# Kernel tuning notes

Hardware: AMD Instinct MI355X
Metric: run time of the kernel (lower is better)

The kernel has to match this reference:

```python
import jax, jax.numpy as jnp
import numpy as np

I, H = 4, 64


def setup_inputs() -> dict:
    key = jax.random.key(0)
    ks = jax.random.split(key, 7)
    s_ih = 1.0 / np.sqrt(H)
    return {
        "x": jax.random.normal(ks[0], (8192, 512, I), dtype=jnp.float32),
        "W_ih": jax.random.uniform(ks[1], (4 * H, I), minval=-s_ih, maxval=s_ih, dtype=jnp.float32),
        "W_hh": jax.random.uniform(ks[2], (4 * H, H), minval=-s_ih, maxval=s_ih, dtype=jnp.float32),
        "b_ih": jax.random.uniform(ks[3], (4 * H,), minval=-s_ih, maxval=s_ih, dtype=jnp.float32),
        "b_hh": jax.random.uniform(ks[4], (4 * H,), minval=-s_ih, maxval=s_ih, dtype=jnp.float32),
        "W_fc": jax.random.uniform(ks[5], (1, H), minval=-s_ih, maxval=s_ih, dtype=jnp.float32),
        "b_fc": jax.random.uniform(ks[6], (1,), minval=-s_ih, maxval=s_ih, dtype=jnp.float32),
    }


def _lstm_last_hidden(x, W_ih, W_hh, b_ih, b_hh):
    # x: [B, T, I] batch_first; PyTorch gate order: i, f, g, o
    B = x.shape[0]
    # Precompute input projections for all timesteps in one GEMM: [T, B, 4H]
    xg = jnp.einsum('bti,gi->tbg', x, W_ih) + (b_ih + b_hh)

    def step(carry, xg_t):
        h, c = carry
        gates = xg_t + h @ W_hh.T  # [B, 4H]
        i, f, g, o = jnp.split(gates, 4, axis=-1)
        i = jax.nn.sigmoid(i)
        f = jax.nn.sigmoid(f)
        g = jnp.tanh(g)
        o = jax.nn.sigmoid(o)
        c = f * c + i * g
        h = o * jnp.tanh(c)
        return (h, c), None

    h0 = jnp.zeros((B, W_hh.shape[1]), dtype=x.dtype)
    c0 = jnp.zeros_like(h0)
    (h_n, _), _ = jax.lax.scan(step, (h0, c0), xg)
    return h_n  # [B, H]


def reference(x, W_ih, W_hh, b_ih, b_hh, W_fc, b_fc):
    h_n = _lstm_last_hidden(x, W_ih, W_hh, b_ih, b_hh)
    return h_n @ W_fc.T + b_fc  # [B, 1]
```

## Files before the change

### kernel.cpp

```cpp
#include <hip/hip_runtime.h>


typedef float f32x4 __attribute__((ext_vector_type(4)));
typedef _Float16 f16x8 __attribute__((ext_vector_type(8)));
typedef _Float16 f16x4 __attribute__((ext_vector_type(4)));

#define TSEQ 512
#define IDIM 4
#define BPB 16
#define TCH 32
#define NCH (TSEQ / TCH)
#define L2E 1.44269504088896340736f

#if __has_builtin(__builtin_amdgcn_exp2f)
#define EX2(v) __builtin_amdgcn_exp2f(v)
#else
#define EX2(v) exp2f(v)
#endif
#define RCP(v) __builtin_amdgcn_rcpf(v)

#define STEP_BARRIER() do {                                   \
    asm volatile("s_waitcnt lgkmcnt(0)" ::: "memory");        \
    __builtin_amdgcn_s_barrier();                             \
} while (0)

__global__ __launch_bounds__(256, 2) void lstm_fused(
    const float* __restrict__ x,
    const float* __restrict__ W_ih,
    const float* __restrict__ W_hh,
    const float* __restrict__ b_ih,
    const float* __restrict__ b_hh,
    const float* __restrict__ W_fc,
    const float* __restrict__ b_fc,
    float* __restrict__ out)
{
    __shared__ __align__(16) _Float16 hbuf[2][BPB * 64];
    __shared__ __align__(16) f16x4    xstage[2][BPB][33];

    const int tid  = threadIdx.x;
    const int lane = tid & 63;
    const int wv   = tid >> 6;
    const int b0   = blockIdx.x * BPB;
    const int r    = lane & 15;
    const int g16  = lane >> 4;

    f16x8 bfrag[4][3];
    #pragma unroll
    for (int t4 = 0; t4 < 4; ++t4) {
        const float sc = (t4 == 2) ? 2.0f * L2E : L2E;
        const int g = t4 * 64 + wv * 16 + r;
        #pragma unroll
        for (int ks = 0; ks < 2; ++ks) {
            const float* p = W_hh + g * 64 + ks * 32 + g16 * 8;
            f16x8 f;
            #pragma unroll
            for (int j = 0; j < 8; ++j) f[j] = (_Float16)(p[j] * sc);
            bfrag[t4][ks] = f;
        }
        f16x8 f;
        #pragma unroll
        for (int j = 0; j < 8; ++j) f[j] = (_Float16)0.0f;
        if (g16 == 0) {
            #pragma unroll
            for (int j = 0; j < 4; ++j) f[j] = (_Float16)(W_ih[g * IDIM + j] * sc);
            float biasf = (b_ih[g] + b_hh[g]) * sc;
            _Float16 hi = (_Float16)biasf;
            f[4] = hi;
            f[5] = (_Float16)(biasf - (float)hi);
        }
        bfrag[t4][2] = f;
    }
    const float wfc = W_fc[lane];
    const float bfc = b_fc[0];
    const f32x4 zero4 = {0.f, 0.f, 0.f, 0.f};

    float c_reg[4] = {0.f, 0.f, 0.f, 0.f};
    for (int i = tid; i < BPB * 64; i += 256) hbuf[0][i] = (_Float16)0.0f;

    const int bb0 = tid >> 5, tf = tid & 31;
    const float* xg0 = x + ((size_t)(b0 + bb0)     * TSEQ + tf) * IDIM;
    const float* xg1 = x + ((size_t)(b0 + bb0 + 8) * TSEQ + tf) * IDIM;
    float4 xn0 = *(const float4*)xg0;
    float4 xn1 = *(const float4*)xg1;
    {
        f16x4 s0, s1;
        s0[0] = (_Float16)xn0.x; s0[1] = (_Float16)xn0.y;
        s0[2] = (_Float16)xn0.z; s0[3] = (_Float16)xn0.w;
        s1[0] = (_Float16)xn1.x; s1[1] = (_Float16)xn1.y;
        s1[2] = (_Float16)xn1.z; s1[3] = (_Float16)xn1.w;
        xstage[0][bb0][tf]     = s0;
        xstage[0][bb0 + 8][tf] = s1;
    }
    __syncthreads();
    xn0 = *(const float4*)(xg0 + TCH * IDIM);
    xn1 = *(const float4*)(xg1 + TCH * IDIM);

    if (((blockIdx.x ^ (blockIdx.x >> 8)) & 1) != 0)
        __builtin_amdgcn_s_sleep(13);

    const int hbase = r * 128;
    const int hs0 = ((g16 + 0) << 4) ^ ((r & 7) << 4);
    const int hs1 = ((g16 + 4) << 4) ^ ((r & 7) << 4);
    int hw[4];
    #pragma unroll
    for (int q = 0; q < 4; ++q) {
        const int bat = 4 * g16 + q;
        hw[q] = (bat * 128 + (wv * 16 + r) * 2) ^ ((bat & 7) << 4);
    }
    char* hbB = (char*)&hbuf[0][0];
    const char* xsB = (const char*)&xstage[0][0][0];
    const int xrow = r * 33 * 8;

    auto substep = [&](int t, int P) {
        const char* rb = hbB + P * 2048;
        char*       wb = hbB + (P ^ 1) * 2048;
        f16x8 a0 = *(const f16x8*)(rb + hbase + hs0);
        f16x8 a1 = *(const f16x8*)(rb + hbase + hs1);
        f16x4 xv = *(const f16x4*)(xsB + ((t >> 5) & 1) * 4224 + xrow + (t & 31) * 8);
        f16x8 ax;
        ax[0] = xv[0]; ax[1] = xv[1]; ax[2] = xv[2]; ax[3] = xv[3];
        ax[4] = (_Float16)1.0f; ax[5] = (_Float16)1.0f;
        ax[6] = (_Float16)0.0f; ax[7] = (_Float16)0.0f;

        f32x4 acc[4];
        __builtin_amdgcn_s_setprio(1);
        #pragma unroll
        for (int t4 = 0; t4 < 4; ++t4) {
            f32x4 a;
            a = __builtin_amdgcn_mfma_f32_16x16x32_f16(a0, bfrag[t4][0], zero4, 0, 0, 0);
            a = __builtin_amdgcn_mfma_f32_16x16x32_f16(a1, bfrag[t4][1], a, 0, 0, 0);
            a = __builtin_amdgcn_mfma_f32_16x16x32_f16(ax, bfrag[t4][2], a, 0, 0, 0);
            acc[t4] = a;
        }
        __builtin_amdgcn_s_setprio(0);

        #pragma unroll
        for (int q = 0; q < 4; ++q) {
            float ei = EX2(-acc[0][q]);
            float ef = EX2(-acc[1][q]);
            float eg = EX2(-acc[2][q]);
            float eo = EX2(-acc[3][q]);
            float A  = 1.f + ei, F = 1.f + ef;
            float Gp = 1.f + eg, Gm = 1.f - eg;
            float P2  = A * Gp;
            float num = c_reg[q] * P2 + Gm * F;
            float c   = num * RCP(P2 * F);
            c_reg[q] = c;
            float uc = fminf(fmaxf(c * (2.0f * L2E), -60.f), 60.f);
            float et = EX2(-uc);
            float h  = (1.f - et) * RCP((1.f + eo) * (1.f + et));
            *(_Float16*)(wb + hw[q]) = (_Float16)h;
        }
        STEP_BARRIER();
    };

    for (int t = 0; t < TSEQ; t += 2) {
        if ((t & (TCH - 1)) == 16) {
            const int c = t >> 5;
            if (c + 1 < NCH) {
                f16x4 s0, s1;
                s0[0] = (_Float16)xn0.x; s0[1] = (_Float16)xn0.y;
                s0[2] = (_Float16)xn0.z; s0[3] = (_Float16)xn0.w;
                s1[0] = (_Float16)xn1.x; s1[1] = (_Float16)xn1.y;
                s1[2] = (_Float16)xn1.z; s1[3] = (_Float16)xn1.w;
                f16x4* dst = &xstage[(c + 1) & 1][0][0];
                dst[bb0 * 33 + tf]       = s0;
                dst[(bb0 + 8) * 33 + tf] = s1;
                if (c + 2 < NCH) {
                    xn0 = *(const float4*)(xg0 + (size_t)(c + 2) * TCH * IDIM);
                    xn1 = *(const float4*)(xg1 + (size_t)(c + 2) * TCH * IDIM);
                }
            }
        }
        substep(t,     0);
        substep(t + 1, 1);
    }

    #pragma unroll
    for (int q = 0; q < 4; ++q) {
        const int bat  = wv * 4 + q;
        const int byte = (bat * 128 + lane * 2) ^ ((bat & 7) << 4);
        float hv = (float)*(const _Float16*)(hbB + byte);
        float partial = hv * wfc;
        #pragma unroll
        for (int off = 32; off > 0; off >>= 1)
            partial += __shfl_down(partial, off);
        if (lane == 0) out[b0 + bat] = partial + bfc;
    }
}

extern "C" void kernel_launch(void* const* d_in, const int* in_sizes, int n_in,
                              void* d_out, int out_size, void* d_ws, size_t ws_size,
                              hipStream_t stream) {
    const float* x    = (const float*)d_in[0];
    const float* W_ih = (const float*)d_in[1];
    const float* W_hh = (const float*)d_in[2];
    const float* b_ih = (const float*)d_in[3];
    const float* b_hh = (const float*)d_in[4];
    const float* W_fc = (const float*)d_in[5];
    const float* b_fc = (const float*)d_in[6];
    float* out = (float*)d_out;

    const int B = in_sizes[0] / (TSEQ * IDIM);
    lstm_fused<<<B / BPB, 256, 0, stream>>>(x, W_ih, W_hh, b_ih, b_hh, W_fc, b_fc, out);
}
```

Measured before the change: 323.9 us.

## Replace LDS x staging with per-lane register prefetch ring and pack cell math

Removes the shared-memory x staging buffer and its periodic chunk copy. Each lane now keeps an 8-deep register ring of float4 x values that it loads straight from global memory, prefetching RING steps ahead. The cell-update math is rewritten with 2-wide float vectors so the compiler can emit packed FP32 ops. In exchange, every step issues a global load per lane that four waves make redundantly, register pressure rises, and the upper clamp on the tanh argument is dropped.

```diff
diff --git a/kernel.cpp b/kernel.cpp
--- a/kernel.cpp
+++ b/kernel.cpp
@@ -2,14 +2,13 @@
 
 
 typedef float f32x4 __attribute__((ext_vector_type(4)));
+typedef float f32x2 __attribute__((ext_vector_type(2)));
 typedef _Float16 f16x8 __attribute__((ext_vector_type(8)));
-typedef _Float16 f16x4 __attribute__((ext_vector_type(4)));
 
 #define TSEQ 512
 #define IDIM 4
 #define BPB 16
-#define TCH 32
-#define NCH (TSEQ / TCH)
+#define RING 8
 #define L2E 1.44269504088896340736f
 
 #if __has_builtin(__builtin_amdgcn_exp2f)
@@ -35,7 +34,6 @@
     float* __restrict__ out)
 {
     __shared__ __align__(16) _Float16 hbuf[2][BPB * 64];
-    __shared__ __align__(16) f16x4    xstage[2][BPB][33];
 
     const int tid  = threadIdx.x;
     const int lane = tid & 63;
@@ -77,23 +75,13 @@
     float c_reg[4] = {0.f, 0.f, 0.f, 0.f};
     for (int i = tid; i < BPB * 64; i += 256) hbuf[0][i] = (_Float16)0.0f;
 
-    const int bb0 = tid >> 5, tf = tid & 31;
-    const float* xg0 = x + ((size_t)(b0 + bb0)     * TSEQ + tf) * IDIM;
-    const float* xg1 = x + ((size_t)(b0 + bb0 + 8) * TSEQ + tf) * IDIM;
-    float4 xn0 = *(const float4*)xg0;
-    float4 xn1 = *(const float4*)xg1;
-    {
-        f16x4 s0, s1;
-        s0[0] = (_Float16)xn0.x; s0[1] = (_Float16)xn0.y;
-        s0[2] = (_Float16)xn0.z; s0[3] = (_Float16)xn0.w;
-        s1[0] = (_Float16)xn1.x; s1[1] = (_Float16)xn1.y;
-        s1[2] = (_Float16)xn1.z; s1[3] = (_Float16)xn1.w;
-        xstage[0][bb0][tf]     = s0;
-        xstage[0][bb0 + 8][tf] = s1;
-    }
+    const float* xgp = x + (size_t)(b0 + r) * (TSEQ * IDIM);
+    float4 xring[RING];
+    #pragma unroll
+    for (int j = 0; j < RING; ++j)
+        xring[j] = *(const float4*)(xgp + j * IDIM);
+
     __syncthreads();
-    xn0 = *(const float4*)(xg0 + TCH * IDIM);
-    xn1 = *(const float4*)(xg1 + TCH * IDIM);
 
     if (((blockIdx.x ^ (blockIdx.x >> 8)) & 1) != 0)
         __builtin_amdgcn_s_sleep(13);
@@ -108,17 +96,58 @@
         hw[q] = (bat * 128 + (wv * 16 + r) * 2) ^ ((bat & 7) << 4);
     }
     char* hbB = (char*)&hbuf[0][0];
-    const char* xsB = (const char*)&xstage[0][0][0];
-    const int xrow = r * 33 * 8;
-
-    auto substep = [&](int t, int P) {
+
+    auto cellquad = [&](const f32x4* acc, char* wb) {
+        const f32x2 one = {1.f, 1.f};
+        f32x2 ei[2], ef[2], eg[2], eo[2];
+        #pragma unroll
+        for (int p = 0; p < 2; ++p) {
+            const int q0 = 2 * p, q1 = 2 * p + 1;
+            ei[p][0] = EX2(-acc[0][q0]); ei[p][1] = EX2(-acc[0][q1]);
+            ef[p][0] = EX2(-acc[1][q0]); ef[p][1] = EX2(-acc[1][q1]);
+            eg[p][0] = EX2(-acc[2][q0]); eg[p][1] = EX2(-acc[2][q1]);
+            eo[p][0] = EX2(-acc[3][q0]); eo[p][1] = EX2(-acc[3][q1]);
+        }
+        f32x2 num[2], rd[2];
+        #pragma unroll
+        for (int p = 0; p < 2; ++p) {
+            f32x2 A  = one + ei[p], F = one + ef[p];
+            f32x2 Gp = one + eg[p], Gm = one - eg[p];
+            f32x2 P2 = A * Gp;
+            f32x2 cr = { c_reg[2 * p], c_reg[2 * p + 1] };
+            num[p] = cr * P2 + Gm * F;
+            f32x2 den = P2 * F;
+            rd[p][0] = RCP(den[0]); rd[p][1] = RCP(den[1]);
+        }
+        f32x2 et[2];
+        #pragma unroll
+        for (int p = 0; p < 2; ++p) {
+            f32x2 c = num[p] * rd[p];
+            c_reg[2 * p]     = c[0];
+            c_reg[2 * p + 1] = c[1];
+            f32x2 uc = __builtin_elementwise_max(c * (2.0f * L2E),
+                                                 f32x2{-60.f, -60.f});
+            et[p][0] = EX2(-uc[0]); et[p][1] = EX2(-uc[1]);
+        }
+        #pragma unroll
+        for (int p = 0; p < 2; ++p) {
+            f32x2 hd = (one + eo[p]) * (one + et[p]);
+            f32x2 rh; rh[0] = RCP(hd[0]); rh[1] = RCP(hd[1]);
+            f32x2 h = (one - et[p]) * rh;
+            *(_Float16*)(wb + hw[2 * p])     = (_Float16)h[0];
+            *(_Float16*)(wb + hw[2 * p + 1]) = (_Float16)h[1];
+        }
+    };
+
+    auto substep = [&](int t, int P, int slot) {
         const char* rb = hbB + P * 2048;
         char*       wb = hbB + (P ^ 1) * 2048;
         f16x8 a0 = *(const f16x8*)(rb + hbase + hs0);
         f16x8 a1 = *(const f16x8*)(rb + hbase + hs1);
-        f16x4 xv = *(const f16x4*)(xsB + ((t >> 5) & 1) * 4224 + xrow + (t & 31) * 8);
+        float4 xf = xring[slot];
         f16x8 ax;
-        ax[0] = xv[0]; ax[1] = xv[1]; ax[2] = xv[2]; ax[3] = xv[3];
+        ax[0] = (_Float16)xf.x; ax[1] = (_Float16)xf.y;
+        ax[2] = (_Float16)xf.z; ax[3] = (_Float16)xf.w;
         ax[4] = (_Float16)1.0f; ax[5] = (_Float16)1.0f;
         ax[6] = (_Float16)0.0f; ax[7] = (_Float16)0.0f;
 
@@ -134,46 +163,20 @@
         }
         __builtin_amdgcn_s_setprio(0);
 
-        #pragma unroll
-        for (int q = 0; q < 4; ++q) {
-            float ei = EX2(-acc[0][q]);
-            float ef = EX2(-acc[1][q]);
-            float eg = EX2(-acc[2][q]);
-            float eo = EX2(-acc[3][q]);
-            float A  = 1.f + ei, F = 1.f + ef;
-            float Gp = 1.f + eg, Gm = 1.f - eg;
-            float P2  = A * Gp;
-            float num = c_reg[q] * P2 + Gm * F;
-            float c   = num * RCP(P2 * F);
-            c_reg[q] = c;
-            float uc = fminf(fmaxf(c * (2.0f * L2E), -60.f), 60.f);
-            float et = EX2(-uc);
-            float h  = (1.f - et) * RCP((1.f + eo) * (1.f + et));
-            *(_Float16*)(wb + hw[q]) = (_Float16)h;
-        }
+        {
+            int tn = t + RING;
+            if (tn > TSEQ - 1) tn = TSEQ - 1;
+            xring[slot] = *(const float4*)(xgp + (size_t)tn * IDIM);
+        }
+
+        cellquad(acc, wb);
         STEP_BARRIER();
     };
 
-    for (int t = 0; t < TSEQ; t += 2) {
-        if ((t & (TCH - 1)) == 16) {
-            const int c = t >> 5;
-            if (c + 1 < NCH) {
-                f16x4 s0, s1;
-                s0[0] = (_Float16)xn0.x; s0[1] = (_Float16)xn0.y;
-                s0[2] = (_Float16)xn0.z; s0[3] = (_Float16)xn0.w;
-                s1[0] = (_Float16)xn1.x; s1[1] = (_Float16)xn1.y;
-                s1[2] = (_Float16)xn1.z; s1[3] = (_Float16)xn1.w;
-                f16x4* dst = &xstage[(c + 1) & 1][0][0];
-                dst[bb0 * 33 + tf]       = s0;
-                dst[(bb0 + 8) * 33 + tf] = s1;
-                if (c + 2 < NCH) {
-                    xn0 = *(const float4*)(xg0 + (size_t)(c + 2) * TCH * IDIM);
-                    xn1 = *(const float4*)(xg1 + (size_t)(c + 2) * TCH * IDIM);
-                }
-            }
-        }
-        substep(t,     0);
-        substep(t + 1, 1);
+    for (int t = 0; t < TSEQ; t += RING) {
+        #pragma unroll
+        for (int j = 0; j < RING; ++j)
+            substep(t + j, j & 1, j);
     }
 
     #pragma unroll
```

New measurement: 291.5 us. -10.0%, faster.
